# Optimization experiments

Hardware: AMD Instinct MI355X
Metric: run time of the kernel (lower is better)

Reference implementation:

```python
import jax, jax.numpy as jnp
import numpy as np

N_GAUSSIANS = 16
B, D = 32768, 64
LOG_2PI = float(np.log(2.0 * np.pi))


def setup_inputs() -> dict:
    key = jax.random.key(0)
    k1, k2, k3, k4 = jax.random.split(key, 4)
    means = jax.random.normal(k1, (B, N_GAUSSIANS * D), dtype=jnp.float32)
    # strictly positive diagonal variances in [0.5, 1.5)
    covs = jax.random.uniform(k2, (B, N_GAUSSIANS * D), dtype=jnp.float32) + 0.5
    # positive mixture weights (softmax-normalized, like a typical MDN head)
    weights = jax.nn.softmax(jax.random.normal(k3, (B, N_GAUSSIANS), dtype=jnp.float32), axis=-1)
    targets = jax.random.normal(k4, (B, D), dtype=jnp.float32)
    return {"means": means, "covs": covs, "weights": weights, "targets": targets}


def reference(means, covs, weights, targets):
    b = means.shape[0]
    mu = means.reshape(b, N_GAUSSIANS, -1)   # [B, K, D]
    var = covs.reshape(b, N_GAUSSIANS, -1)   # [B, K, D]
    t = targets[:, None, :]                  # [B, 1, D]
    d = mu.shape[-1]
    # analytic diagonal-Gaussian log-prob (same math as MultivariateNormal
    # with diag_embed covariance, without the Cholesky)
    quad = jnp.sum((t - mu) ** 2 / var, axis=-1)          # [B, K]
    logdet = jnp.sum(jnp.log(var), axis=-1)               # [B, K]
    log_probs = -0.5 * (d * LOG_2PI + logdet + quad)      # [B, K]
    log_probs = jnp.clip(log_probs, -100.0, 0.0)
    log_probs_weighted = log_probs + jnp.log(weights)
    total_log_likelihood = jax.nn.logsumexp(log_probs_weighted, axis=1)  # [B]
    return -1.0 * total_log_likelihood
```

## Files before the change

kernel.cpp:

```cpp
#include <hip/hip_runtime.h>
#include <math.h>

#define NG 16
#define DIM 64
#define LOG_2PI 1.8378770664093453f

__global__ __launch_bounds__(256) void gmm_loss_kernel(
    const float* __restrict__ means,
    const float* __restrict__ covs,
    const float* __restrict__ weights,
    const float* __restrict__ targets,
    float* __restrict__ out, int B)
{
    const int wave = threadIdx.x >> 6;
    const int lane = threadIdx.x & 63;
    const int b = blockIdx.x * 4 + wave;
    if (b >= B) return;

    const int q = lane >> 4;
    const int dpart = lane & 15;

    const float4* t4 = (const float4*)(targets + (size_t)b * DIM);
    const float4 t = t4[dpart];

    const float4* m4 = (const float4*)(means + (size_t)b * (NG * DIM));
    const float4* v4 = (const float4*)(covs  + (size_t)b * (NG * DIM));

    float s[4];
#pragma unroll
    for (int kb = 0; kb < 4; ++kb) {
        const float4 m = m4[kb * 64 + lane];
        const float4 v = v4[kb * 64 + lane];
        float dx = t.x - m.x;
        float p = dx * dx * __builtin_amdgcn_rcpf(v.x) + __logf(v.x);
        dx = t.y - m.y;
        p += dx * dx * __builtin_amdgcn_rcpf(v.y) + __logf(v.y);
        dx = t.z - m.z;
        p += dx * dx * __builtin_amdgcn_rcpf(v.z) + __logf(v.z);
        dx = t.w - m.w;
        p += dx * dx * __builtin_amdgcn_rcpf(v.w) + __logf(v.w);
        p += __shfl_xor(p, 1);
        p += __shfl_xor(p, 2);
        p += __shfl_xor(p, 4);
        p += __shfl_xor(p, 8);
        s[kb] = p;
    }

    float lpw[4];
#pragma unroll
    for (int kb = 0; kb < 4; ++kb) {
        float lp = -0.5f * (DIM * LOG_2PI + s[kb]);
        lp = fminf(fmaxf(lp, -100.0f), 0.0f);
        const float w = weights[(size_t)b * NG + kb * 4 + q];
        lpw[kb] = lp + __logf(w);
    }

    float M = fmaxf(fmaxf(lpw[0], lpw[1]), fmaxf(lpw[2], lpw[3]));
    M = fmaxf(M, __shfl_xor(M, 16));
    M = fmaxf(M, __shfl_xor(M, 32));
    float sm = __expf(lpw[0] - M) + __expf(lpw[1] - M) +
               __expf(lpw[2] - M) + __expf(lpw[3] - M);
    sm += __shfl_xor(sm, 16);
    sm += __shfl_xor(sm, 32);

    if (lane == 0) {
        out[b] = -(M + __logf(sm));
    }
}

extern "C" void kernel_launch(void* const* d_in, const int* in_sizes, int n_in,
                              void* d_out, int out_size, void* d_ws, size_t ws_size,
                              hipStream_t stream) {
    const float* means   = (const float*)d_in[0];
    const float* covs    = (const float*)d_in[1];
    const float* weights = (const float*)d_in[2];
    const float* targets = (const float*)d_in[3];
    float* out = (float*)d_out;

    const int B = in_sizes[0] / (NG * DIM);
    const int rows_per_block = 4;
    const int grid = (B + rows_per_block - 1) / rows_per_block;
    gmm_loss_kernel<<<grid, 256, 0, stream>>>(means, covs, weights, targets, out, B);
}
```

Measured before the change: 282.6 us.

## Map one batch row per 256-thread block with LDS cross-wave logsumexp

Each block now handles a single batch row, with each thread loading one float4 of means and covs, instead of each wave handling a row across four unrolled iterations. Per-Gaussian partial sums pass through shared memory and a barrier so one wave can do the logsumexp. The four logs per thread are merged into a single log of a product. This gives more blocks and fewer loads per thread, but adds a __syncthreads and LDS traffic per row and leaves three waves idle during the final reduction.

```diff
diff --git a/kernel.cpp b/kernel.cpp
--- a/kernel.cpp
+++ b/kernel.cpp
@@ -10,61 +10,59 @@
     const float* __restrict__ covs,
     const float* __restrict__ weights,
     const float* __restrict__ targets,
-    float* __restrict__ out, int B)
+    float* __restrict__ out)
 {
-    const int wave = threadIdx.x >> 6;
-    const int lane = threadIdx.x & 63;
-    const int b = blockIdx.x * 4 + wave;
-    if (b >= B) return;
+    const int b = blockIdx.x;
+    const int tid = threadIdx.x;
+    const int lane = tid & 63;
 
-    const int q = lane >> 4;
-    const int dpart = lane & 15;
-
-    const float4* t4 = (const float4*)(targets + (size_t)b * DIM);
-    const float4 t = t4[dpart];
+    __shared__ float sbuf[NG];
 
     const float4* m4 = (const float4*)(means + (size_t)b * (NG * DIM));
     const float4* v4 = (const float4*)(covs  + (size_t)b * (NG * DIM));
+    const float4* t4 = (const float4*)(targets + (size_t)b * DIM);
 
-    float s[4];
-#pragma unroll
-    for (int kb = 0; kb < 4; ++kb) {
-        const float4 m = m4[kb * 64 + lane];
-        const float4 v = v4[kb * 64 + lane];
-        float dx = t.x - m.x;
-        float p = dx * dx * __builtin_amdgcn_rcpf(v.x) + __logf(v.x);
-        dx = t.y - m.y;
-        p += dx * dx * __builtin_amdgcn_rcpf(v.y) + __logf(v.y);
-        dx = t.z - m.z;
-        p += dx * dx * __builtin_amdgcn_rcpf(v.z) + __logf(v.z);
-        dx = t.w - m.w;
-        p += dx * dx * __builtin_amdgcn_rcpf(v.w) + __logf(v.w);
-        p += __shfl_xor(p, 1);
-        p += __shfl_xor(p, 2);
-        p += __shfl_xor(p, 4);
-        p += __shfl_xor(p, 8);
-        s[kb] = p;
-    }
+    const float4 m = m4[tid];
+    const float4 v = v4[tid];
+    const float4 t = t4[tid & 15];
 
-    float lpw[4];
-#pragma unroll
-    for (int kb = 0; kb < 4; ++kb) {
-        float lp = -0.5f * (DIM * LOG_2PI + s[kb]);
+    float dx = t.x - m.x;
+    float p  = dx * dx * __builtin_amdgcn_rcpf(v.x);
+    dx = t.y - m.y;
+    p += dx * dx * __builtin_amdgcn_rcpf(v.y);
+    dx = t.z - m.z;
+    p += dx * dx * __builtin_amdgcn_rcpf(v.z);
+    dx = t.w - m.w;
+    p += dx * dx * __builtin_amdgcn_rcpf(v.w);
+    p += __logf(v.x * v.y * v.z * v.w);
+
+    p += __shfl_xor(p, 1);
+    p += __shfl_xor(p, 2);
+    p += __shfl_xor(p, 4);
+    p += __shfl_xor(p, 8);
+
+    if ((lane & 15) == 0) sbuf[tid >> 4] = p;
+    __syncthreads();
+
+    if (tid < 64) {
+        const int g = lane & 15;
+        const float s = sbuf[g];
+        float lp = -0.5f * (DIM * LOG_2PI + s);
         lp = fminf(fmaxf(lp, -100.0f), 0.0f);
-        const float w = weights[(size_t)b * NG + kb * 4 + q];
-        lpw[kb] = lp + __logf(w);
-    }
+        const float lw = lp + __logf(weights[(size_t)b * NG + g]);
 
-    float M = fmaxf(fmaxf(lpw[0], lpw[1]), fmaxf(lpw[2], lpw[3]));
-    M = fmaxf(M, __shfl_xor(M, 16));
-    M = fmaxf(M, __shfl_xor(M, 32));
-    float sm = __expf(lpw[0] - M) + __expf(lpw[1] - M) +
-               __expf(lpw[2] - M) + __expf(lpw[3] - M);
-    sm += __shfl_xor(sm, 16);
-    sm += __shfl_xor(sm, 32);
+        float M = lw;
+        M = fmaxf(M, __shfl_xor(M, 1));
+        M = fmaxf(M, __shfl_xor(M, 2));
+        M = fmaxf(M, __shfl_xor(M, 4));
+        M = fmaxf(M, __shfl_xor(M, 8));
+        float e = __expf(lw - M);
+        e += __shfl_xor(e, 1);
+        e += __shfl_xor(e, 2);
+        e += __shfl_xor(e, 4);
+        e += __shfl_xor(e, 8);
 
-    if (lane == 0) {
-        out[b] = -(M + __logf(sm));
+        if (tid == 0) out[b] = -(M + __logf(e));
     }
 }
 
@@ -78,7 +76,5 @@
     float* out = (float*)d_out;
 
     const int B = in_sizes[0] / (NG * DIM);
-    const int rows_per_block = 4;
-    const int grid = (B + rows_per_block - 1) / rows_per_block;
-    gmm_loss_kernel<<<grid, 256, 0, stream>>>(means, covs, weights, targets, out, B);
+    gmm_loss_kernel<<<B, 256, 0, stream>>>(means, covs, weights, targets, out);
 }
```

Measured after the change: 273.1 us. 3.4% less time.

## Use persistent grid-stride waves with double-buffered row prefetch

Applied to the files above, without the earlier changes.

Switches from one wave per row to a fixed grid of 1024 blocks where each wave strides over rows and prefetches the next row into registers while computing the current one. It also merges the four per-element logs into a single log of the product, and batches the shuffle reductions across the four component groups. The aim is to hide global memory latency in a bandwidth-bound kernel and cut transcendental work. The cost is higher register use, which may lower occupancy, and the product of variances could lose some precision.

```diff
diff --git a/kernel.cpp b/kernel.cpp
--- a/kernel.cpp
+++ b/kernel.cpp
@@ -4,68 +4,112 @@
 #define NG 16
 #define DIM 64
 #define LOG_2PI 1.8378770664093453f
+#define WPB 4
 
-__global__ __launch_bounds__(256) void gmm_loss_kernel(
+
+struct Row {
+    float4 m0, m1, m2, m3;
+    float4 v0, v1, v2, v3;
+    float4 t;
+    float  w0, w1, w2, w3;
+};
+
+__device__ __forceinline__ void load_row(const float* __restrict__ means,
+                                         const float* __restrict__ covs,
+                                         const float* __restrict__ targets,
+                                         const float* __restrict__ weights,
+                                         size_t b, int lane, int dpart, int q,
+                                         Row& r)
+{
+    const float4* m4 = (const float4*)(means + b * (size_t)(NG * DIM));
+    const float4* v4 = (const float4*)(covs  + b * (size_t)(NG * DIM));
+    r.m0 = m4[lane];        r.v0 = v4[lane];
+    r.m1 = m4[64  + lane];  r.v1 = v4[64  + lane];
+    r.m2 = m4[128 + lane];  r.v2 = v4[128 + lane];
+    r.m3 = m4[192 + lane];  r.v3 = v4[192 + lane];
+    r.t  = ((const float4*)(targets + b * DIM))[dpart];
+    const float* wrow = weights + b * NG;
+    r.w0 = wrow[q];
+    r.w1 = wrow[4  + q];
+    r.w2 = wrow[8  + q];
+    r.w3 = wrow[12 + q];
+}
+
+__device__ __forceinline__ float part(const float4 m, const float4 v, const float4 t)
+{
+    float dx = t.x - m.x;
+    float p  = dx * dx * __builtin_amdgcn_rcpf(v.x);
+    dx = t.y - m.y; p += dx * dx * __builtin_amdgcn_rcpf(v.y);
+    dx = t.z - m.z; p += dx * dx * __builtin_amdgcn_rcpf(v.z);
+    dx = t.w - m.w; p += dx * dx * __builtin_amdgcn_rcpf(v.w);
+    p += __logf(v.x * v.y * v.z * v.w);
+    return p;
+}
+
+__device__ __forceinline__ void process_row(const Row& r,
+                                            float* __restrict__ out,
+                                            size_t b, int lane)
+{
+    float s0 = part(r.m0, r.v0, r.t);
+    float s1 = part(r.m1, r.v1, r.t);
+    float s2 = part(r.m2, r.v2, r.t);
+    float s3 = part(r.m3, r.v3, r.t);
+#pragma unroll
+    for (int st = 1; st < 16; st <<= 1) {
+        s0 += __shfl_xor(s0, st);
+        s1 += __shfl_xor(s1, st);
+        s2 += __shfl_xor(s2, st);
+        s3 += __shfl_xor(s3, st);
+    }
+    const float c = -0.5f * (DIM * LOG_2PI);
+    float l0 = fminf(fmaxf(c - 0.5f * s0, -100.0f), 0.0f) + __logf(r.w0);
+    float l1 = fminf(fmaxf(c - 0.5f * s1, -100.0f), 0.0f) + __logf(r.w1);
+    float l2 = fminf(fmaxf(c - 0.5f * s2, -100.0f), 0.0f) + __logf(r.w2);
+    float l3 = fminf(fmaxf(c - 0.5f * s3, -100.0f), 0.0f) + __logf(r.w3);
+
+    float M = fmaxf(fmaxf(l0, l1), fmaxf(l2, l3));
+    M = fmaxf(M, __shfl_xor(M, 16));
+    M = fmaxf(M, __shfl_xor(M, 32));
+    float e = __expf(l0 - M) + __expf(l1 - M) + __expf(l2 - M) + __expf(l3 - M);
+    e += __shfl_xor(e, 16);
+    e += __shfl_xor(e, 32);
+
+    if (lane == 0) out[b] = -(M + __logf(e));
+}
+
+__global__ __launch_bounds__(256, 4) void gmm_loss_kernel(
     const float* __restrict__ means,
     const float* __restrict__ covs,
     const float* __restrict__ weights,
     const float* __restrict__ targets,
-    float* __restrict__ out, int B)
+    float* __restrict__ out, int B, int stride)
 {
-    const int wave = threadIdx.x >> 6;
-    const int lane = threadIdx.x & 63;
-    const int b = blockIdx.x * 4 + wave;
-    if (b >= B) return;
-
-    const int q = lane >> 4;
+    const int wave_id = blockIdx.x * WPB + (threadIdx.x >> 6);
+    const int lane  = threadIdx.x & 63;
+    const int q     = lane >> 4;
     const int dpart = lane & 15;
 
-    const float4* t4 = (const float4*)(targets + (size_t)b * DIM);
-    const float4 t = t4[dpart];
+    size_t b = (size_t)wave_id;
+    if (b >= (size_t)B) return;
 
-    const float4* m4 = (const float4*)(means + (size_t)b * (NG * DIM));
-    const float4* v4 = (const float4*)(covs  + (size_t)b * (NG * DIM));
+    Row A, C;
+    load_row(means, covs, targets, weights, b, lane, dpart, q, A);
+    size_t bn = b + stride;
 
-    float s[4];
-#pragma unroll
-    for (int kb = 0; kb < 4; ++kb) {
-        const float4 m = m4[kb * 64 + lane];
-        const float4 v = v4[kb * 64 + lane];
-        float dx = t.x - m.x;
-        float p = dx * dx * __builtin_amdgcn_rcpf(v.x) + __logf(v.x);
-        dx = t.y - m.y;
-        p += dx * dx * __builtin_amdgcn_rcpf(v.y) + __logf(v.y);
-        dx = t.z - m.z;
-        p += dx * dx * __builtin_amdgcn_rcpf(v.z) + __logf(v.z);
-        dx = t.w - m.w;
-        p += dx * dx * __builtin_amdgcn_rcpf(v.w) + __logf(v.w);
-        p += __shfl_xor(p, 1);
-        p += __shfl_xor(p, 2);
-        p += __shfl_xor(p, 4);
-        p += __shfl_xor(p, 8);
-        s[kb] = p;
+    while (bn < (size_t)B) {
+        load_row(means, covs, targets, weights, bn, lane, dpart, q, C);
+        process_row(A, out, b, lane);
+        b = bn; bn += stride;
+        if (bn < (size_t)B) {
+            load_row(means, covs, targets, weights, bn, lane, dpart, q, A);
+            process_row(C, out, b, lane);
+            b = bn; bn += stride;
+        } else {
+            process_row(C, out, b, lane);
+            return;
+        }
     }
-
-    float lpw[4];
-#pragma unroll
-    for (int kb = 0; kb < 4; ++kb) {
-        float lp = -0.5f * (DIM * LOG_2PI + s[kb]);
-        lp = fminf(fmaxf(lp, -100.0f), 0.0f);
-        const float w = weights[(size_t)b * NG + kb * 4 + q];
-        lpw[kb] = lp + __logf(w);
-    }
-
-    float M = fmaxf(fmaxf(lpw[0], lpw[1]), fmaxf(lpw[2], lpw[3]));
-    M = fmaxf(M, __shfl_xor(M, 16));
-    M = fmaxf(M, __shfl_xor(M, 32));
-    float sm = __expf(lpw[0] - M) + __expf(lpw[1] - M) +
-               __expf(lpw[2] - M) + __expf(lpw[3] - M);
-    sm += __shfl_xor(sm, 16);
-    sm += __shfl_xor(sm, 32);
-
-    if (lane == 0) {
-        out[b] = -(M + __logf(sm));
-    }
+    process_row(A, out, b, lane);
 }
 
 extern "C" void kernel_launch(void* const* d_in, const int* in_sizes, int n_in,
@@ -78,7 +122,9 @@
     float* out = (float*)d_out;
 
     const int B = in_sizes[0] / (NG * DIM);
-    const int rows_per_block = 4;
-    const int grid = (B + rows_per_block - 1) / rows_per_block;
-    gmm_loss_kernel<<<grid, 256, 0, stream>>>(means, covs, weights, targets, out, B);
+    int blocks = 1024;
+    if (blocks * WPB > B) blocks = (B + WPB - 1) / WPB;
+    const int stride = blocks * WPB;
+    gmm_loss_kernel<<<blocks, 256, 0, stream>>>(means, covs, weights, targets,
+                                                out, B, stride);
 }
```

After: 293.2 us. 3.8% more time.
